# Performance work log

Hardware: AMD Instinct MI355X
Metric: run time of the kernel (lower is better)

The kernel has to match this reference:

```python
import jax, jax.numpy as jnp
import numpy as np

N_NODES = 100000
N_EDGES = 3200000
HID = 52
N_LAYERS = 3


def setup_inputs() -> dict:
    key = jax.random.key(0)
    ks = jax.random.split(key, 6)
    x = jax.random.normal(ks[0], (N_NODES, HID), dtype=jnp.float32)
    edge_index = jax.random.randint(ks[1], (2, N_EDGES), 0, N_NODES, dtype=jnp.int32)
    w1 = jax.random.normal(ks[2], (N_LAYERS, HID, 2 * HID), dtype=jnp.float32) * 0.1
    b1 = jnp.zeros((N_LAYERS, 2 * HID), dtype=jnp.float32)
    w2 = jax.random.normal(ks[3], (N_LAYERS, 2 * HID, HID), dtype=jnp.float32) * 0.1
    b2 = jnp.zeros((N_LAYERS, HID), dtype=jnp.float32)
    eps = jnp.zeros((N_LAYERS,), dtype=jnp.float32)
    lin_w = jax.random.normal(ks[4], (HID * (N_LAYERS + 1), HID), dtype=jnp.float32) * 0.1
    lin_b = jnp.zeros((HID,), dtype=jnp.float32)
    return {"x": x, "edge_index": edge_index, "w1": w1, "b1": b1,
            "w2": w2, "b2": b2, "eps": eps, "lin_w": lin_w, "lin_b": lin_b}


def reference(x, edge_index, w1, b1, w2, b2, eps, lin_w, lin_b):
    src, dst = edge_index[0], edge_index[1]
    n = x.shape[0]
    h = x
    h_list = [x]
    for l in range(N_LAYERS):
        # GINConv: sum-aggregate neighbor features at target nodes
        agg = jax.ops.segment_sum(h[src], dst, num_segments=n)  # [N, HID]
        z = (1.0 + eps[l]) * h + agg
        # 2-layer MLP: Linear -> ReLU -> Linear
        z = jnp.maximum(z @ w1[l] + b1[l], 0.0) @ w2[l] + b2[l]
        # outer ReLU (dropout p=0 is identity)
        h = jnp.maximum(z, 0.0)
        h_list.append(h)
    node_repr = jnp.concatenate(h_list, axis=1)  # [N, HID*(L+1)]
    return node_repr @ lin_w + lin_b
```

## Files before the change

### kernel.cpp

```cpp
#include <hip/hip_runtime.h>

#define HID 52
#define HID2 104
#define P1_CHUNK 8192
#define NBIN_MAX 512
#define HSTRIDE 136
#define BINCAP 10240
#define SR_STRIDE 14336

typedef unsigned short ushort_t;
typedef unsigned int uint_t;
typedef short bf16x8 __attribute__((ext_vector_type(8)));
typedef float f32x4 __attribute__((ext_vector_type(4)));
typedef float f32x2 __attribute__((ext_vector_type(2)));

__device__ __forceinline__ ushort_t f2bf(float f) {
    union { float f; uint_t u; } c; c.f = f;
    uint_t u = c.u + 0x7FFFu + ((c.u >> 16) & 1u);
    return (ushort_t)(u >> 16);
}
__device__ __forceinline__ float bflo(uint_t u) {
    union { uint_t u; float f; } c; c.u = u << 16; return c.f;
}
__device__ __forceinline__ float bfhi(uint_t u) {
    union { uint_t u; float f; } c; c.u = u & 0xFFFF0000u; return c.f;
}
__device__ __forceinline__ f32x2 rawpair(uint_t a, uint_t b) {
    union { uint_t u; float f; } ca, cb; ca.u = a; cb.u = b;
    return (f32x2){ca.f, cb.f};
}
__device__ __forceinline__ f32x2 shlpair(uint_t a, uint_t b) {
    union { uint_t u; float f; } ca, cb; ca.u = a << 16; cb.u = b << 16;
    return (f32x2){ca.f, cb.f};
}
__device__ __forceinline__ void pkacc(f32x2& a, f32x2 b) {
    asm("v_pk_add_f32 %0, %0, %1" : "+v"(a) : "v"(b));
}
template<int IMM>
__device__ __forceinline__ f32x2 swz2(f32x2 v) {
    union { float f; int i; } a, b; a.f = v.x; b.f = v.y;
    int ra = __builtin_amdgcn_ds_swizzle(a.i, IMM);
    int rb = __builtin_amdgcn_ds_swizzle(b.i, IMM);
    union { int i; float f; } c, d; c.i = ra; d.i = rb;
    return (f32x2){c.f, d.f};
}

__global__ __launch_bounds__(256) void setup_kernel(const float* __restrict__ x,
                                                    const float* __restrict__ w1,
                                                    const float* __restrict__ w2,
                                                    const float* __restrict__ lin_w,
                                                    ushort_t* __restrict__ xb,
                                                    ushort_t* __restrict__ h1b,
                                                    ushort_t* __restrict__ h2b,
                                                    ushort_t* __restrict__ w1f,
                                                    ushort_t* __restrict__ w2f,
                                                    ushort_t* __restrict__ linf,
                                                    int* __restrict__ gcnt,
                                                    int n, int nxblk) {
    int blk = blockIdx.x;
    int tid = threadIdx.x;
    if (blk < nxblk) {
        int t = blk * 256 + tid;
        if (t >= n * 16) return;
        int node = t >> 4, pp = t & 15;
        int c0 = pp * 4;
        ushort_t o[4];
#pragma unroll
        for (int j = 0; j < 4; j++) {
            int c = c0 + j;
            o[j] = (c < HID) ? f2bf(x[(size_t)node * HID + c]) : 0;
        }
        uint_t u0 = (uint_t)o[0] | ((uint_t)o[1] << 16);
        uint_t u1 = (uint_t)o[2] | ((uint_t)o[3] << 16);
        *(uint2*)(xb + (size_t)node * 64 + c0) = make_uint2(u0, u1);
        return;
    }
    if (blk == nxblk) {
        gcnt[tid] = 0; gcnt[tid + 256] = 0;
        ushort_t* arr = (tid < 64) ? xb : (tid < 128) ? h1b : h2b;
        arr[(size_t)n * 64 + (tid & 63)] = 0;
        return;
    }
    int gid = (blk - nxblk - 1) * 4 + (tid >> 6);
    int lane = tid & 63;
    if (gid >= 122) return;
    int m = lane & 15, q = lane >> 4;
    ushort_t o[8];
    ushort_t* dstp;
    if (gid < 42) {
        int l = gid / 14, r = gid % 14, ct = r >> 1, ks = r & 1;
        int nn = ct * 16 + m;
#pragma unroll
        for (int j = 0; j < 8; j++) {
            int k = ks * 32 + q * 8 + j;
            o[j] = (k < HID && nn < HID2) ? f2bf(w1[((size_t)l * HID + k) * HID2 + nn]) : 0;
        }
        dstp = w1f + ((size_t)(l * 14 + ct * 2 + ks) * 64 + lane) * 8;
    } else if (gid < 90) {
        int g2 = gid - 42, l = g2 / 16, r = g2 % 16, ct = r >> 2, ks = r & 3;
        int nn = ct * 16 + m;
#pragma unroll
        for (int j = 0; j < 8; j++) {
            int k = ks * 32 + q * 8 + j;
            o[j] = (k < HID2 && nn < HID) ? f2bf(w2[((size_t)l * HID2 + k) * HID + nn]) : 0;
        }
        dstp = w2f + ((size_t)(l * 16 + ct * 4 + ks) * 64 + lane) * 8;
    } else {
        int g2 = gid - 90, ct = g2 >> 3, ks = g2 & 7;
        int nn = ct * 16 + m;
#pragma unroll
        for (int j = 0; j < 8; j++) {
            int kg = ks * 32 + q * 8 + j;
            int seg = kg >> 6, kk = kg & 63;
            o[j] = (kk < HID && nn < HID) ? f2bf(lin_w[((size_t)seg * HID + kk) * HID + nn]) : 0;
        }
        dstp = linf + ((size_t)(ct * 8 + ks) * 64 + lane) * 8;
    }
    uint4 u;
    u.x = (uint_t)o[0] | ((uint_t)o[1] << 16);
    u.y = (uint_t)o[2] | ((uint_t)o[3] << 16);
    u.z = (uint_t)o[4] | ((uint_t)o[5] << 16);
    u.w = (uint_t)o[6] | ((uint_t)o[7] << 16);
    *(uint4*)dstp = u;
}

__global__ __launch_bounds__(256) void pass1_kernel(const int* __restrict__ src,
                                                    const int* __restrict__ dst,
                                                    int* __restrict__ gcnt,
                                                    uint_t* __restrict__ packed, int E) {
    __shared__ uint_t stage[P1_CHUNK];
    __shared__ ushort_t sbin[P1_CHUNK];
    __shared__ int cnt[NBIN_MAX];
    __shared__ int curs[NBIN_MAX];
    __shared__ int diff[NBIN_MAX];
    __shared__ int wsum[4];
    int tid = threadIdx.x;
    int lane = tid & 63, wv = tid >> 6;
    int b0 = 2 * tid, b1 = 2 * tid + 1;
    cnt[b0] = 0; cnt[b1] = 0;
    __syncthreads();
    int base = blockIdx.x * P1_CHUNK;
    int cend = min(P1_CHUNK, E - base);
    int nq = cend >> 2;
    const uint4* d4p = (const uint4*)(dst + base);
    const uint4* s4p = (const uint4*)(src + base);
    for (int j = tid; j < nq; j += 256) {
        uint4 d = d4p[j];
        atomicAdd(&cnt[d.x >> 8], 1);
        atomicAdd(&cnt[d.y >> 8], 1);
        atomicAdd(&cnt[d.z >> 8], 1);
        atomicAdd(&cnt[d.w >> 8], 1);
    }
    for (int i = (nq << 2) + tid; i < cend; i += 256)
        atomicAdd(&cnt[((uint_t)dst[base + i]) >> 8], 1);
    __syncthreads();
    int c0 = cnt[b0], c1 = cnt[b1];
    int pair = c0 + c1;
    int inc = pair;
#pragma unroll
    for (int off = 1; off < 64; off <<= 1) {
        int t = __shfl_up(inc, off);
        if (lane >= off) inc += t;
    }
    if (lane == 63) wsum[wv] = inc;
    __syncthreads();
    int wpre = 0;
#pragma unroll
    for (int i = 0; i < 3; i++) wpre += (i < wv) ? wsum[i] : 0;
    int ex = wpre + inc - pair;
    int s0 = ex, s1 = ex + c0;
    curs[b0] = s0;
    curs[b1] = s1;
    int g0 = c0 ? (b0 * BINCAP + atomicAdd(&gcnt[b0], c0)) : 0;
    int g1 = c1 ? (b1 * BINCAP + atomicAdd(&gcnt[b1], c1)) : 0;
    diff[b0] = g0 - s0;
    diff[b1] = g1 - s1;
    __syncthreads();
    for (int j = tid; j < nq; j += 256) {
        uint4 d = d4p[j];
        uint4 s = s4p[j];
        int b, pos;
        b = d.x >> 8; pos = atomicAdd(&curs[b], 1);
        stage[pos] = (s.x << 8) | (d.x & 255u); sbin[pos] = (ushort_t)b;
        b = d.y >> 8; pos = atomicAdd(&curs[b], 1);
        stage[pos] = (s.y << 8) | (d.y & 255u); sbin[pos] = (ushort_t)b;
        b = d.z >> 8; pos = atomicAdd(&curs[b], 1);
        stage[pos] = (s.z << 8) | (d.z & 255u); sbin[pos] = (ushort_t)b;
        b = d.w >> 8; pos = atomicAdd(&curs[b], 1);
        stage[pos] = (s.w << 8) | (d.w & 255u); sbin[pos] = (ushort_t)b;
    }
    for (int i = (nq << 2) + tid; i < cend; i += 256) {
        uint_t d = (uint_t)dst[base + i];
        uint_t s = (uint_t)src[base + i];
        int b = d >> 8;
        int pos = atomicAdd(&curs[b], 1);
        stage[pos] = (s << 8) | (d & 255u);
        sbin[pos] = (ushort_t)b;
    }
    __syncthreads();
    for (int i = tid; i < cend; i += 256) {
        packed[diff[sbin[i]] + i] = stage[i];
    }
}

__global__ __launch_bounds__(256) void pass2_kernel(const uint_t* __restrict__ packed,
                                                    const int* __restrict__ gcnt,
                                                    int* __restrict__ srcsorted,
                                                    int* __restrict__ nrs,
                                                    int* __restrict__ ndeg, int N) {
    __shared__ int hist[256];
    __shared__ int curs[256];
    __shared__ int wsum[4];
    int b = blockIdx.x;
    int tid = threadIdx.x;
    int lane = tid & 63, wv = tid >> 6;
    hist[tid] = 0;
    __syncthreads();
    int beg = b * BINCAP;
    int cntE = gcnt[b];
    int nq = cntE >> 2;
    const uint4* p4p = (const uint4*)(packed + beg);
    for (int j = tid; j < nq; j += 256) {
        uint4 p = p4p[j];
        atomicAdd(&hist[p.x & 255u], 1);
        atomicAdd(&hist[p.y & 255u], 1);
        atomicAdd(&hist[p.z & 255u], 1);
        atomicAdd(&hist[p.w & 255u], 1);
    }
    for (int i = (nq << 2) + tid; i < cntE; i += 256)
        atomicAdd(&hist[packed[beg + i] & 255u], 1);
    __syncthreads();
    int v = hist[tid];
    int pv = (v + 15) & ~15;
    int inc = pv;
#pragma unroll
    for (int off = 1; off < 64; off <<= 1) {
        int t = __shfl_up(inc, off);
        if (lane >= off) inc += t;
    }
    if (lane == 63) wsum[wv] = inc;
    __syncthreads();
    int wpre = 0;
#pragma unroll
    for (int i = 0; i < 3; i++) wpre += (i < wv) ? wsum[i] : 0;
    int start = b * SR_STRIDE + wpre + inc - pv;
    int node = b * 256 + tid;
    if (node < N) { nrs[node] = start; ndeg[node] = pv; }
    curs[tid] = start;
    __syncthreads();
    for (int j = tid; j < nq; j += 256) {
        uint4 p = p4p[j];
        int pos;
        pos = atomicAdd(&curs[p.x & 255u], 1); srcsorted[pos] = (int)(p.x >> 8);
        pos = atomicAdd(&curs[p.y & 255u], 1); srcsorted[pos] = (int)(p.y >> 8);
        pos = atomicAdd(&curs[p.z & 255u], 1); srcsorted[pos] = (int)(p.z >> 8);
        pos = atomicAdd(&curs[p.w & 255u], 1); srcsorted[pos] = (int)(p.w >> 8);
    }
    for (int i = (nq << 2) + tid; i < cntE; i += 256) {
        uint_t p = packed[beg + i];
        int pos = atomicAdd(&curs[p & 255u], 1);
        srcsorted[pos] = (int)(p >> 8);
    }
    __syncthreads();
    for (int i = start + v; i < start + pv; i++) srcsorted[i] = N;
}

__global__ __launch_bounds__(256) void agg_kernel(const ushort_t* __restrict__ hb,
                                                  const int* __restrict__ nrs,
                                                  const int* __restrict__ ndeg,
                                                  const int* __restrict__ srcsorted,
                                                  const float* __restrict__ eps,
                                                  ushort_t* __restrict__ zb, int n) {
    int wpair = (blockIdx.x * blockDim.x + threadIdx.x) >> 6;
    int lane = threadIdx.x & 63;
    int half = lane >> 5;
    int wid = wpair * 2 + half;
    bool valid = (wid < n);
    int node = valid ? wid : (n - 1);
    int hl = lane & 31;
    int g = hl >> 3;
    int sub = lane & 7;
    int beg = nrs[node];
    int total = valid ? ndeg[node] : 0;
    const char* hc = (const char*)hb;
    const char* sp = (const char*)srcsorted;
    unsigned lbB = (unsigned)sub * 16u;
    unsigned bo = (unsigned)(beg + g) * 4u;

    f32x2 AO0 = {0,0}, AO1 = {0,0}, AE0 = {0,0}, AE1 = {0,0};
    f32x2 BO0 = {0,0}, BO1 = {0,0}, BE0 = {0,0}, BE1 = {0,0};
    if (total > 0) {
        int f0 = *(const int*)(sp + bo);
        int f1 = *(const int*)(sp + bo + 16);
        int f2 = *(const int*)(sp + bo + 32);
        int f3 = *(const int*)(sp + bo + 48);
        int f4 = *(const int*)(sp + bo + 64);
        int f5 = *(const int*)(sp + bo + 80);
        int f6 = *(const int*)(sp + bo + 96);
        int f7 = *(const int*)(sp + bo + 112);
        for (int b = 0; b < total; b += 32) {
            bool ok = (b + 16) < total;
            int e0 = f0, e1 = f1, e2 = f2, e3 = f3;
            int e4 = ok ? f4 : n, e5 = ok ? f5 : n;
            int e6 = ok ? f6 : n, e7 = ok ? f7 : n;
            f0 = *(const int*)(sp + bo + 128);
            f1 = *(const int*)(sp + bo + 144);
            f2 = *(const int*)(sp + bo + 160);
            f3 = *(const int*)(sp + bo + 176);
            f4 = *(const int*)(sp + bo + 192);
            f5 = *(const int*)(sp + bo + 208);
            f6 = *(const int*)(sp + bo + 224);
            f7 = *(const int*)(sp + bo + 240);
            bo += 128;
            uint4 v0 = *(const uint4*)(hc + (((unsigned)e0 << 7) + lbB));
            uint4 v1 = *(const uint4*)(hc + (((unsigned)e1 << 7) + lbB));
            uint4 v2 = *(const uint4*)(hc + (((unsigned)e2 << 7) + lbB));
            uint4 v3 = *(const uint4*)(hc + (((unsigned)e3 << 7) + lbB));
            uint4 v4 = *(const uint4*)(hc + (((unsigned)e4 << 7) + lbB));
            uint4 v5 = *(const uint4*)(hc + (((unsigned)e5 << 7) + lbB));
            uint4 v6 = *(const uint4*)(hc + (((unsigned)e6 << 7) + lbB));
            uint4 v7 = *(const uint4*)(hc + (((unsigned)e7 << 7) + lbB));
            pkacc(AO0, rawpair(v0.x, v0.y)); pkacc(AO1, rawpair(v0.z, v0.w));
            pkacc(AE0, shlpair(v0.x, v0.y)); pkacc(AE1, shlpair(v0.z, v0.w));
            pkacc(BO0, rawpair(v1.x, v1.y)); pkacc(BO1, rawpair(v1.z, v1.w));
            pkacc(BE0, shlpair(v1.x, v1.y)); pkacc(BE1, shlpair(v1.z, v1.w));
            pkacc(AO0, rawpair(v2.x, v2.y)); pkacc(AO1, rawpair(v2.z, v2.w));
            pkacc(AE0, shlpair(v2.x, v2.y)); pkacc(AE1, shlpair(v2.z, v2.w));
            pkacc(BO0, rawpair(v3.x, v3.y)); pkacc(BO1, rawpair(v3.z, v3.w));
            pkacc(BE0, shlpair(v3.x, v3.y)); pkacc(BE1, shlpair(v3.z, v3.w));
            pkacc(AO0, rawpair(v4.x, v4.y)); pkacc(AO1, rawpair(v4.z, v4.w));
            pkacc(AE0, shlpair(v4.x, v4.y)); pkacc(AE1, shlpair(v4.z, v4.w));
            pkacc(BO0, rawpair(v5.x, v5.y)); pkacc(BO1, rawpair(v5.z, v5.w));
            pkacc(BE0, shlpair(v5.x, v5.y)); pkacc(BE1, shlpair(v5.z, v5.w));
            pkacc(AO0, rawpair(v6.x, v6.y)); pkacc(AO1, rawpair(v6.z, v6.w));
            pkacc(AE0, shlpair(v6.x, v6.y)); pkacc(AE1, shlpair(v6.z, v6.w));
            pkacc(BO0, rawpair(v7.x, v7.y)); pkacc(BO1, rawpair(v7.z, v7.w));
            pkacc(BE0, shlpair(v7.x, v7.y)); pkacc(BE1, shlpair(v7.z, v7.w));
        }
    }
    pkacc(AO0, BO0); pkacc(AO1, BO1);
    pkacc(AE0, BE0); pkacc(AE1, BE1);
    pkacc(AO0, swz2<0x201F>(AO0)); pkacc(AO1, swz2<0x201F>(AO1));
    pkacc(AE0, swz2<0x201F>(AE0)); pkacc(AE1, swz2<0x201F>(AE1));
    pkacc(AO0, swz2<0x401F>(AO0)); pkacc(AO1, swz2<0x401F>(AO1));
    pkacc(AE0, swz2<0x401F>(AE0)); pkacc(AE1, swz2<0x401F>(AE1));
    if (hl < 8 && valid) {
        float sc = 1.0f + eps[0];
        uint4 sv = *(const uint4*)(hb + (size_t)wid * 64 + hl * 8);
        float o0 = fmaf(sc, bflo(sv.x), AE0.x), o1 = fmaf(sc, bfhi(sv.x), AO0.x);
        float o2 = fmaf(sc, bflo(sv.y), AE0.y), o3 = fmaf(sc, bfhi(sv.y), AO0.y);
        float o4 = fmaf(sc, bflo(sv.z), AE1.x), o5 = fmaf(sc, bfhi(sv.z), AO1.x);
        float o6 = fmaf(sc, bflo(sv.w), AE1.y), o7 = fmaf(sc, bfhi(sv.w), AO1.y);
        uint4 u;
        u.x = (uint_t)f2bf(o0) | ((uint_t)f2bf(o1) << 16);
        u.y = (uint_t)f2bf(o2) | ((uint_t)f2bf(o3) << 16);
        u.z = (uint_t)f2bf(o4) | ((uint_t)f2bf(o5) << 16);
        u.w = (uint_t)f2bf(o6) | ((uint_t)f2bf(o7) << 16);
        *(uint4*)(zb + (size_t)wid * 64 + hl * 8) = u;
    }
}

template<int LAST>
__global__ __launch_bounds__(256) void mlp_kernel(const ushort_t* __restrict__ zb,
                                                  const ushort_t* __restrict__ w1f,
                                                  const float* __restrict__ b1,
                                                  const ushort_t* __restrict__ w2f,
                                                  const float* __restrict__ b2,
                                                  ushort_t* __restrict__ hbout,
                                                  const ushort_t* __restrict__ xb,
                                                  const ushort_t* __restrict__ h1b,
                                                  const ushort_t* __restrict__ h2b,
                                                  const ushort_t* __restrict__ linf,
                                                  const float* __restrict__ lin_b,
                                                  float* __restrict__ out, int n) {
    __shared__ ushort_t hid[64 * HSTRIDE];
    __shared__ ushort_t h3t[LAST ? 64 * 68 : 1];
    int tid = threadIdx.x;
    int w = tid >> 6, lane = tid & 63, m = lane & 15, q = lane >> 4;
    for (int i = tid; i < 64 * 32; i += 256) {
        int r = i >> 5, c = HID2 + (i & 31);
        hid[r * HSTRIDE + c] = 0;
    }
    __syncthreads();

    int nb = blockIdx.x * 64 + w * 16;
    f32x4 acc1[7];
#pragma unroll
    for (int ct = 0; ct < 7; ct++) {
        int col = ct * 16 + m;
        float bv = (col < HID2) ? b1[col] : 0.f;
        acc1[ct] = (f32x4){bv, bv, bv, bv};
    }
    int anode = min(nb + m, n - 1);
#pragma unroll
    for (int ks = 0; ks < 2; ks++) {
        bf16x8 a = *(const bf16x8*)(zb + (size_t)anode * 64 + ks * 32 + q * 8);
#pragma unroll
        for (int ct = 0; ct < 7; ct++) {
            bf16x8 b = *(const bf16x8*)(w1f + ((size_t)(ct * 2 + ks) * 64 + lane) * 8);
            acc1[ct] = __builtin_amdgcn_mfma_f32_16x16x32_bf16(a, b, acc1[ct], 0, 0, 0);
        }
    }
#pragma unroll
    for (int ct = 0; ct < 7; ct++) {
#pragma unroll
        for (int r = 0; r < 4; r++) {
            float v = fmaxf(acc1[ct][r], 0.f);
            int row = w * 16 + q * 4 + r;
            hid[row * HSTRIDE + ct * 16 + m] = f2bf(v);
        }
    }
    f32x4 acc2[4];
#pragma unroll
    for (int ct = 0; ct < 4; ct++) {
        int col = ct * 16 + m;
        float bv = (col < HID) ? b2[col] : 0.f;
        acc2[ct] = (f32x4){bv, bv, bv, bv};
    }
#pragma unroll
    for (int ks = 0; ks < 4; ks++) {
        bf16x8 a = *(const bf16x8*)&hid[(w * 16 + m) * HSTRIDE + ks * 32 + q * 8];
#pragma unroll
        for (int ct = 0; ct < 4; ct++) {
            bf16x8 b = *(const bf16x8*)(w2f + ((size_t)(ct * 4 + ks) * 64 + lane) * 8);
            acc2[ct] = __builtin_amdgcn_mfma_f32_16x16x32_bf16(a, b, acc2[ct], 0, 0, 0);
        }
    }

    if (!LAST) {
#pragma unroll
        for (int ct = 0; ct < 4; ct++) {
#pragma unroll
            for (int r = 0; r < 4; r++) {
                int node = nb + q * 4 + r;
                if (node < n) {
                    float v = fmaxf(acc2[ct][r], 0.f);
                    hbout[(size_t)node * 64 + ct * 16 + m] = f2bf(v);
                }
            }
        }
    } else {
#pragma unroll
        for (int ct = 0; ct < 4; ct++) {
#pragma unroll
            for (int r = 0; r < 4; r++) {
                float v = fmaxf(acc2[ct][r], 0.f);
                h3t[(w * 16 + q * 4 + r) * 68 + ct * 16 + m] = f2bf(v);
            }
        }
        f32x4 accF[4];
#pragma unroll
        for (int ct = 0; ct < 4; ct++) {
            int col = ct * 16 + m;
            float bv = (col < HID) ? lin_b[col] : 0.f;
            accF[ct] = (f32x4){bv, bv, bv, bv};
        }
        const ushort_t* segs[3] = {xb, h1b, h2b};
#pragma unroll
        for (int ks = 0; ks < 8; ks++) {
            bf16x8 a;
            if (ks < 6) {
                const ushort_t* p = segs[ks >> 1];
                a = *(const bf16x8*)(p + (size_t)anode * 64 + (ks & 1) * 32 + q * 8);
            } else {
                a = *(const bf16x8*)&h3t[(w * 16 + m) * 68 + (ks & 1) * 32 + q * 8];
            }
#pragma unroll
            for (int ct = 0; ct < 4; ct++) {
                bf16x8 b = *(const bf16x8*)(linf + ((size_t)(ct * 8 + ks) * 64 + lane) * 8);
                accF[ct] = __builtin_amdgcn_mfma_f32_16x16x32_bf16(a, b, accF[ct], 0, 0, 0);
            }
        }
#pragma unroll
        for (int ct = 0; ct < 4; ct++) {
            int col = ct * 16 + m;
            if (col < HID) {
#pragma unroll
                for (int r = 0; r < 4; r++) {
                    int node = nb + q * 4 + r;
                    if (node < n)
                        out[(size_t)node * HID + col] = accF[ct][r];
                }
            }
        }
    }
}

extern "C" void kernel_launch(void* const* d_in, const int* in_sizes, int n_in,
                              void* d_out, int out_size, void* d_ws, size_t ws_size,
                              hipStream_t stream) {
    const float* x     = (const float*)d_in[0];
    const int*   ei    = (const int*)d_in[1];
    const float* w1    = (const float*)d_in[2];
    const float* b1    = (const float*)d_in[3];
    const float* w2    = (const float*)d_in[4];
    const float* b2    = (const float*)d_in[5];
    const float* eps   = (const float*)d_in[6];
    const float* lin_w = (const float*)d_in[7];
    const float* lin_b = (const float*)d_in[8];
    float* out = (float*)d_out;

    const int N = in_sizes[0] / HID;
    const int E = in_sizes[1] / 2;
    const int* src = ei;
    const int* dst = ei + E;

    const int NBIN = (N + 255) / 256;

    char* p = (char*)d_ws;
    const size_t ROWS = (size_t)(N + 1) * 64 * 2;
    ushort_t* xb  = (ushort_t*)p;  p += ROWS;
    ushort_t* zb  = (ushort_t*)p;  p += ROWS;
    ushort_t* h1b = (ushort_t*)p;  p += ROWS;
    ushort_t* h2b = (ushort_t*)p;  p += ROWS;
    ushort_t* w1f = (ushort_t*)p;  p += 3 * 14 * 512 * 2;
    ushort_t* w2f = (ushort_t*)p;  p += 3 * 16 * 512 * 2;
    ushort_t* linf= (ushort_t*)p;  p += 32 * 512 * 2;
    int* gcnt     = (int*)p;       p += 512 * 4;
    int* nrs      = (int*)p;       p += (size_t)(N + 4) * 4;
    int* ndeg     = (int*)p;       p += (size_t)(N + 4) * 4;
    int* srcsorted = (int*)p;      p += (size_t)NBIN * SR_STRIDE * 4 + 256;
    uint_t* packed = (uint_t*)zb;

    ushort_t* hbs[3] = {xb, h1b, h2b};

    const int BLK = 256;
    const int NP1 = (E + P1_CHUNK - 1) / P1_CHUNK;
    const int NXBLK = (N * 16 + BLK - 1) / BLK;
    const int NBUCK = (N + 63) / 64;
    const int NPAIR = (N + 1) / 2;
    dim3 blk(BLK);
    dim3 grid_agg(((size_t)NPAIR * 64 + BLK - 1) / BLK);

    setup_kernel<<<NXBLK + 32, blk, 0, stream>>>(x, w1, w2, lin_w,
                                                 xb, h1b, h2b,
                                                 w1f, w2f, linf, gcnt, N, NXBLK);
    pass1_kernel<<<NP1, blk, 0, stream>>>(src, dst, gcnt, packed, E);
    pass2_kernel<<<NBIN, blk, 0, stream>>>(packed, gcnt, srcsorted, nrs, ndeg, N);

    for (int l = 0; l < 2; l++) {
        agg_kernel<<<grid_agg, blk, 0, stream>>>(hbs[l], nrs, ndeg, srcsorted, eps + l, zb, N);
        mlp_kernel<0><<<NBUCK, blk, 0, stream>>>(zb,
                                                 w1f + (size_t)l * 14 * 512,
                                                 b1 + (size_t)l * HID2,
                                                 w2f + (size_t)l * 16 * 512,
                                                 b2 + (size_t)l * HID,
                                                 hbs[l + 1],
                                                 nullptr, nullptr, nullptr,
                                                 nullptr, nullptr, nullptr, N);
    }
    agg_kernel<<<grid_agg, blk, 0, stream>>>(h2b, nrs, ndeg, srcsorted, eps + 2, zb, N);
    mlp_kernel<1><<<NBUCK, blk, 0, stream>>>(zb,
                                             w1f + 2 * 14 * 512,
                                             b1 + 2 * HID2,
                                             w2f + 2 * 16 * 512,
                                             b2 + 2 * HID,
                                             nullptr,
                                             xb, h1b, h2b,
                                             linf, lin_b, out, N);
}
```

Baseline: 353.7 us.

## Merge setup work into pass2 kernel and vectorize input conversion

The separate setup kernel is removed. Its x-to-bf16 conversion, pad-row zeroing and weight repacking now run as extra blocks of the pass2 CSR-building kernel, and gcnt is cleared with a memset. The x conversion now uses float4 loads with 8 columns per thread instead of scalar loads. The MLP kernel issues its A-fragment loads before the LDS zeroing barrier and zeroes the padding with one vectorized store per thread. This removes a launch and lets the independent conversion overlap the sort pass, at the cost of a heavier combined kernel with divergent block roles.

```diff
diff --git a/kernel.cpp b/kernel.cpp
--- a/kernel.cpp
+++ b/kernel.cpp
@@ -43,85 +43,6 @@
     int rb = __builtin_amdgcn_ds_swizzle(b.i, IMM);
     union { int i; float f; } c, d; c.i = ra; d.i = rb;
     return (f32x2){c.f, d.f};
-}
-
-__global__ __launch_bounds__(256) void setup_kernel(const float* __restrict__ x,
-                                                    const float* __restrict__ w1,
-                                                    const float* __restrict__ w2,
-                                                    const float* __restrict__ lin_w,
-                                                    ushort_t* __restrict__ xb,
-                                                    ushort_t* __restrict__ h1b,
-                                                    ushort_t* __restrict__ h2b,
-                                                    ushort_t* __restrict__ w1f,
-                                                    ushort_t* __restrict__ w2f,
-                                                    ushort_t* __restrict__ linf,
-                                                    int* __restrict__ gcnt,
-                                                    int n, int nxblk) {
-    int blk = blockIdx.x;
-    int tid = threadIdx.x;
-    if (blk < nxblk) {
-        int t = blk * 256 + tid;
-        if (t >= n * 16) return;
-        int node = t >> 4, pp = t & 15;
-        int c0 = pp * 4;
-        ushort_t o[4];
-#pragma unroll
-        for (int j = 0; j < 4; j++) {
-            int c = c0 + j;
-            o[j] = (c < HID) ? f2bf(x[(size_t)node * HID + c]) : 0;
-        }
-        uint_t u0 = (uint_t)o[0] | ((uint_t)o[1] << 16);
-        uint_t u1 = (uint_t)o[2] | ((uint_t)o[3] << 16);
-        *(uint2*)(xb + (size_t)node * 64 + c0) = make_uint2(u0, u1);
-        return;
-    }
-    if (blk == nxblk) {
-        gcnt[tid] = 0; gcnt[tid + 256] = 0;
-        ushort_t* arr = (tid < 64) ? xb : (tid < 128) ? h1b : h2b;
-        arr[(size_t)n * 64 + (tid & 63)] = 0;
-        return;
-    }
-    int gid = (blk - nxblk - 1) * 4 + (tid >> 6);
-    int lane = tid & 63;
-    if (gid >= 122) return;
-    int m = lane & 15, q = lane >> 4;
-    ushort_t o[8];
-    ushort_t* dstp;
-    if (gid < 42) {
-        int l = gid / 14, r = gid % 14, ct = r >> 1, ks = r & 1;
-        int nn = ct * 16 + m;
-#pragma unroll
-        for (int j = 0; j < 8; j++) {
-            int k = ks * 32 + q * 8 + j;
-            o[j] = (k < HID && nn < HID2) ? f2bf(w1[((size_t)l * HID + k) * HID2 + nn]) : 0;
-        }
-        dstp = w1f + ((size_t)(l * 14 + ct * 2 + ks) * 64 + lane) * 8;
-    } else if (gid < 90) {
-        int g2 = gid - 42, l = g2 / 16, r = g2 % 16, ct = r >> 2, ks = r & 3;
-        int nn = ct * 16 + m;
-#pragma unroll
-        for (int j = 0; j < 8; j++) {
-            int k = ks * 32 + q * 8 + j;
-            o[j] = (k < HID2 && nn < HID) ? f2bf(w2[((size_t)l * HID2 + k) * HID + nn]) : 0;
-        }
-        dstp = w2f + ((size_t)(l * 16 + ct * 4 + ks) * 64 + lane) * 8;
-    } else {
-        int g2 = gid - 90, ct = g2 >> 3, ks = g2 & 7;
-        int nn = ct * 16 + m;
-#pragma unroll
-        for (int j = 0; j < 8; j++) {
-            int kg = ks * 32 + q * 8 + j;
-            int seg = kg >> 6, kk = kg & 63;
-            o[j] = (kk < HID && nn < HID) ? f2bf(lin_w[((size_t)seg * HID + kk) * HID + nn]) : 0;
-        }
-        dstp = linf + ((size_t)(ct * 8 + ks) * 64 + lane) * 8;
-    }
-    uint4 u;
-    u.x = (uint_t)o[0] | ((uint_t)o[1] << 16);
-    u.y = (uint_t)o[2] | ((uint_t)o[3] << 16);
-    u.z = (uint_t)o[4] | ((uint_t)o[5] << 16);
-    u.w = (uint_t)o[6] | ((uint_t)o[7] << 16);
-    *(uint4*)dstp = u;
 }
 
 __global__ __launch_bounds__(256) void pass1_kernel(const int* __restrict__ src,
@@ -203,66 +124,147 @@
     }
 }
 
-__global__ __launch_bounds__(256) void pass2_kernel(const uint_t* __restrict__ packed,
-                                                    const int* __restrict__ gcnt,
-                                                    int* __restrict__ srcsorted,
-                                                    int* __restrict__ nrs,
-                                                    int* __restrict__ ndeg, int N) {
+__global__ __launch_bounds__(256) void mid_kernel(const uint_t* __restrict__ packed,
+                                                  const int* __restrict__ gcnt,
+                                                  int* __restrict__ srcsorted,
+                                                  int* __restrict__ nrs,
+                                                  int* __restrict__ ndeg,
+                                                  const float* __restrict__ x,
+                                                  const float* __restrict__ w1,
+                                                  const float* __restrict__ w2,
+                                                  const float* __restrict__ lin_w,
+                                                  ushort_t* __restrict__ xb,
+                                                  ushort_t* __restrict__ h1b,
+                                                  ushort_t* __restrict__ h2b,
+                                                  ushort_t* __restrict__ w1f,
+                                                  ushort_t* __restrict__ w2f,
+                                                  ushort_t* __restrict__ linf,
+                                                  int N, int nbin, int nconv) {
     __shared__ int hist[256];
     __shared__ int curs[256];
     __shared__ int wsum[4];
-    int b = blockIdx.x;
+    int blk = blockIdx.x;
     int tid = threadIdx.x;
-    int lane = tid & 63, wv = tid >> 6;
-    hist[tid] = 0;
-    __syncthreads();
-    int beg = b * BINCAP;
-    int cntE = gcnt[b];
-    int nq = cntE >> 2;
-    const uint4* p4p = (const uint4*)(packed + beg);
-    for (int j = tid; j < nq; j += 256) {
-        uint4 p = p4p[j];
-        atomicAdd(&hist[p.x & 255u], 1);
-        atomicAdd(&hist[p.y & 255u], 1);
-        atomicAdd(&hist[p.z & 255u], 1);
-        atomicAdd(&hist[p.w & 255u], 1);
-    }
-    for (int i = (nq << 2) + tid; i < cntE; i += 256)
-        atomicAdd(&hist[packed[beg + i] & 255u], 1);
-    __syncthreads();
-    int v = hist[tid];
-    int pv = (v + 15) & ~15;
-    int inc = pv;
-#pragma unroll
-    for (int off = 1; off < 64; off <<= 1) {
-        int t = __shfl_up(inc, off);
-        if (lane >= off) inc += t;
-    }
-    if (lane == 63) wsum[wv] = inc;
-    __syncthreads();
-    int wpre = 0;
-#pragma unroll
-    for (int i = 0; i < 3; i++) wpre += (i < wv) ? wsum[i] : 0;
-    int start = b * SR_STRIDE + wpre + inc - pv;
-    int node = b * 256 + tid;
-    if (node < N) { nrs[node] = start; ndeg[node] = pv; }
-    curs[tid] = start;
-    __syncthreads();
-    for (int j = tid; j < nq; j += 256) {
-        uint4 p = p4p[j];
-        int pos;
-        pos = atomicAdd(&curs[p.x & 255u], 1); srcsorted[pos] = (int)(p.x >> 8);
-        pos = atomicAdd(&curs[p.y & 255u], 1); srcsorted[pos] = (int)(p.y >> 8);
-        pos = atomicAdd(&curs[p.z & 255u], 1); srcsorted[pos] = (int)(p.z >> 8);
-        pos = atomicAdd(&curs[p.w & 255u], 1); srcsorted[pos] = (int)(p.w >> 8);
-    }
-    for (int i = (nq << 2) + tid; i < cntE; i += 256) {
-        uint_t p = packed[beg + i];
-        int pos = atomicAdd(&curs[p & 255u], 1);
-        srcsorted[pos] = (int)(p >> 8);
-    }
-    __syncthreads();
-    for (int i = start + v; i < start + pv; i++) srcsorted[i] = N;
+    if (blk < nbin) {
+        int b = blk;
+        int lane = tid & 63, wv = tid >> 6;
+        hist[tid] = 0;
+        __syncthreads();
+        int beg = b * BINCAP;
+        int cntE = gcnt[b];
+        int nq = cntE >> 2;
+        const uint4* p4p = (const uint4*)(packed + beg);
+        for (int j = tid; j < nq; j += 256) {
+            uint4 p = p4p[j];
+            atomicAdd(&hist[p.x & 255u], 1);
+            atomicAdd(&hist[p.y & 255u], 1);
+            atomicAdd(&hist[p.z & 255u], 1);
+            atomicAdd(&hist[p.w & 255u], 1);
+        }
+        for (int i = (nq << 2) + tid; i < cntE; i += 256)
+            atomicAdd(&hist[packed[beg + i] & 255u], 1);
+        __syncthreads();
+        int v = hist[tid];
+        int pv = (v + 15) & ~15;
+        int inc = pv;
+#pragma unroll
+        for (int off = 1; off < 64; off <<= 1) {
+            int t = __shfl_up(inc, off);
+            if (lane >= off) inc += t;
+        }
+        if (lane == 63) wsum[wv] = inc;
+        __syncthreads();
+        int wpre = 0;
+#pragma unroll
+        for (int i = 0; i < 3; i++) wpre += (i < wv) ? wsum[i] : 0;
+        int start = b * SR_STRIDE + wpre + inc - pv;
+        int node = b * 256 + tid;
+        if (node < N) { nrs[node] = start; ndeg[node] = pv; }
+        curs[tid] = start;
+        __syncthreads();
+        for (int j = tid; j < nq; j += 256) {
+            uint4 p = p4p[j];
+            int pos;
+            pos = atomicAdd(&curs[p.x & 255u], 1); srcsorted[pos] = (int)(p.x >> 8);
+            pos = atomicAdd(&curs[p.y & 255u], 1); srcsorted[pos] = (int)(p.y >> 8);
+            pos = atomicAdd(&curs[p.z & 255u], 1); srcsorted[pos] = (int)(p.z >> 8);
+            pos = atomicAdd(&curs[p.w & 255u], 1); srcsorted[pos] = (int)(p.w >> 8);
+        }
+        for (int i = (nq << 2) + tid; i < cntE; i += 256) {
+            uint_t p = packed[beg + i];
+            int pos = atomicAdd(&curs[p & 255u], 1);
+            srcsorted[pos] = (int)(p >> 8);
+        }
+        __syncthreads();
+        for (int i = start + v; i < start + pv; i++) srcsorted[i] = N;
+        return;
+    }
+    if (blk < nbin + nconv) {
+        int t = (blk - nbin) * 256 + tid;
+        if (t >= N * 8) return;
+        int node = t >> 3, pp = t & 7, c0 = pp * 8;
+        uint4 u = make_uint4(0, 0, 0, 0);
+        if (c0 < 48) {
+            float4 xa = *(const float4*)(x + (size_t)node * HID + c0);
+            float4 xc = *(const float4*)(x + (size_t)node * HID + c0 + 4);
+            u.x = (uint_t)f2bf(xa.x) | ((uint_t)f2bf(xa.y) << 16);
+            u.y = (uint_t)f2bf(xa.z) | ((uint_t)f2bf(xa.w) << 16);
+            u.z = (uint_t)f2bf(xc.x) | ((uint_t)f2bf(xc.y) << 16);
+            u.w = (uint_t)f2bf(xc.z) | ((uint_t)f2bf(xc.w) << 16);
+        } else if (c0 == 48) {
+            float4 xa = *(const float4*)(x + (size_t)node * HID + 48);
+            u.x = (uint_t)f2bf(xa.x) | ((uint_t)f2bf(xa.y) << 16);
+            u.y = (uint_t)f2bf(xa.z) | ((uint_t)f2bf(xa.w) << 16);
+        }
+        *(uint4*)(xb + (size_t)node * 64 + c0) = u;
+        return;
+    }
+    if (blk == nbin + nconv) {
+        ushort_t* arr = (tid < 64) ? xb : (tid < 128) ? h1b : h2b;
+        arr[(size_t)N * 64 + (tid & 63)] = 0;
+        return;
+    }
+    int gid = (blk - nbin - nconv - 1) * 4 + (tid >> 6);
+    int lane = tid & 63;
+    if (gid >= 122) return;
+    int m = lane & 15, q = lane >> 4;
+    ushort_t o[8];
+    ushort_t* dstp;
+    if (gid < 42) {
+        int l = gid / 14, r = gid % 14, ct = r >> 1, ks = r & 1;
+        int nn = ct * 16 + m;
+#pragma unroll
+        for (int j = 0; j < 8; j++) {
+            int k = ks * 32 + q * 8 + j;
+            o[j] = (k < HID && nn < HID2) ? f2bf(w1[((size_t)l * HID + k) * HID2 + nn]) : 0;
+        }
+        dstp = w1f + ((size_t)(l * 14 + ct * 2 + ks) * 64 + lane) * 8;
+    } else if (gid < 90) {
+        int g2 = gid - 42, l = g2 / 16, r = g2 % 16, ct = r >> 2, ks = r & 3;
+        int nn = ct * 16 + m;
+#pragma unroll
+        for (int j = 0; j < 8; j++) {
+            int k = ks * 32 + q * 8 + j;
+            o[j] = (k < HID2 && nn < HID) ? f2bf(w2[((size_t)l * HID2 + k) * HID + nn]) : 0;
+        }
+        dstp = w2f + ((size_t)(l * 16 + ct * 4 + ks) * 64 + lane) * 8;
+    } else {
+        int g2 = gid - 90, ct = g2 >> 3, ks = g2 & 7;
+        int nn = ct * 16 + m;
+#pragma unroll
+        for (int j = 0; j < 8; j++) {
+            int kg = ks * 32 + q * 8 + j;
+            int seg = kg >> 6, kk = kg & 63;
+            o[j] = (kk < HID && nn < HID) ? f2bf(lin_w[((size_t)seg * HID + kk) * HID + nn]) : 0;
+        }
+        dstp = linf + ((size_t)(ct * 8 + ks) * 64 + lane) * 8;
+    }
+    uint4 u;
+    u.x = (uint_t)o[0] | ((uint_t)o[1] << 16);
+    u.y = (uint_t)o[2] | ((uint_t)o[3] << 16);
+    u.z = (uint_t)o[4] | ((uint_t)o[5] << 16);
+    u.w = (uint_t)o[6] | ((uint_t)o[7] << 16);
+    *(uint4*)dstp = u;
 }
 
 __global__ __launch_bounds__(256) void agg_kernel(const ushort_t* __restrict__ hb,
@@ -377,13 +379,15 @@
     __shared__ ushort_t h3t[LAST ? 64 * 68 : 1];
     int tid = threadIdx.x;
     int w = tid >> 6, lane = tid & 63, m = lane & 15, q = lane >> 4;
-    for (int i = tid; i < 64 * 32; i += 256) {
-        int r = i >> 5, c = HID2 + (i & 31);
-        hid[r * HSTRIDE + c] = 0;
-    }
+    int nb = blockIdx.x * 64 + w * 16;
+    int anode = min(nb + m, n - 1);
+    bf16x8 afr[2];
+    afr[0] = *(const bf16x8*)(zb + (size_t)anode * 64 + q * 8);
+    afr[1] = *(const bf16x8*)(zb + (size_t)anode * 64 + 32 + q * 8);
+    *(uint4*)((char*)hid + (size_t)(tid >> 2) * 272 + 208 + (size_t)(tid & 3) * 16)
+        = make_uint4(0, 0, 0, 0);
     __syncthreads();
 
-    int nb = blockIdx.x * 64 + w * 16;
     f32x4 acc1[7];
 #pragma unroll
     for (int ct = 0; ct < 7; ct++) {
@@ -391,14 +395,12 @@
         float bv = (col < HID2) ? b1[col] : 0.f;
         acc1[ct] = (f32x4){bv, bv, bv, bv};
     }
-    int anode = min(nb + m, n - 1);
 #pragma unroll
     for (int ks = 0; ks < 2; ks++) {
-        bf16x8 a = *(const bf16x8*)(zb + (size_t)anode * 64 + ks * 32 + q * 8);
 #pragma unroll
         for (int ct = 0; ct < 7; ct++) {
             bf16x8 b = *(const bf16x8*)(w1f + ((size_t)(ct * 2 + ks) * 64 + lane) * 8);
-            acc1[ct] = __builtin_amdgcn_mfma_f32_16x16x32_bf16(a, b, acc1[ct], 0, 0, 0);
+            acc1[ct] = __builtin_amdgcn_mfma_f32_16x16x32_bf16(afr[ks], b, acc1[ct], 0, 0, 0);
         }
     }
 #pragma unroll
@@ -526,17 +528,19 @@
 
     const int BLK = 256;
     const int NP1 = (E + P1_CHUNK - 1) / P1_CHUNK;
-    const int NXBLK = (N * 16 + BLK - 1) / BLK;
+    const int NCONV = (N * 8 + BLK - 1) / BLK;
     const int NBUCK = (N + 63) / 64;
     const int NPAIR = (N + 1) / 2;
     dim3 blk(BLK);
     dim3 grid_agg(((size_t)NPAIR * 64 + BLK - 1) / BLK);
 
-    setup_kernel<<<NXBLK + 32, blk, 0, stream>>>(x, w1, w2, lin_w,
-                                                 xb, h1b, h2b,
-                                                 w1f, w2f, linf, gcnt, N, NXBLK);
+    hipMemsetAsync(gcnt, 0, 512 * sizeof(int), stream);
     pass1_kernel<<<NP1, blk, 0, stream>>>(src, dst, gcnt, packed, E);
-    pass2_kernel<<<NBIN, blk, 0, stream>>>(packed, gcnt, srcsorted, nrs, ndeg, N);
+    mid_kernel<<<NBIN + NCONV + 1 + 31, blk, 0, stream>>>(packed, gcnt, srcsorted, nrs, ndeg,
+                                                          x, w1, w2, lin_w,
+                                                          xb, h1b, h2b,
+                                                          w1f, w2f, linf,
+                                                          N, NBIN, NCONV);
 
     for (int l = 0; l < 2; l++) {
         agg_kernel<<<grid_agg, blk, 0, stream>>>(hbs[l], nrs, ndeg, srcsorted, eps + l, zb, N);
```

After: 346.6 us. -2.0%, faster.
